# Kernel optimization log

Measured on AMD Instinct MI355X. Metric: run time of the kernel, lower is better.

## Reference

```python
import jax, jax.numpy as jnp
import numpy as np

B, T, D, H = 8, 1024, 768, 12
HD = D // H  # 64
EPS = 1e-5


def setup_inputs() -> dict:
    key = jax.random.key(0)
    ks = jax.random.split(key, 16)
    s = lambda fan_in: 1.0 / np.sqrt(fan_in)
    inp = {
        "x": jax.random.normal(ks[0], (B, T, D), jnp.float32),
        # per-head Q/K/V projections stacked: [H, D, HD]
        "wq": jax.random.normal(ks[1], (H, D, HD), jnp.float32) * s(D),
        "bq": jnp.zeros((H, HD), jnp.float32),
        "wk": jax.random.normal(ks[2], (H, D, HD), jnp.float32) * s(D),
        "bk": jnp.zeros((H, HD), jnp.float32),
        "wv": jax.random.normal(ks[3], (H, D, HD), jnp.float32) * s(D),
        "bv": jnp.zeros((H, HD), jnp.float32),
        "w_proj": jax.random.normal(ks[4], (D, D), jnp.float32) * s(D),
        "b_proj": jnp.zeros((D,), jnp.float32),
        "g1": jnp.ones((D,), jnp.float32),
        "be1": jnp.zeros((D,), jnp.float32),
        "g2": jnp.ones((D,), jnp.float32),
        "be2": jnp.zeros((D,), jnp.float32),
        "w_fc": jax.random.normal(ks[5], (D, 4 * D), jnp.float32) * s(D),
        "b_fc": jnp.zeros((4 * D,), jnp.float32),
        "w_cp": jax.random.normal(ks[6], (4 * D, D), jnp.float32) * s(4 * D),
        "b_cp": jnp.zeros((D,), jnp.float32),
    }
    return inp


def _layernorm(x, g, b):
    mu = jnp.mean(x, axis=-1, keepdims=True)
    var = jnp.var(x, axis=-1, keepdims=True)
    return (x - mu) * jax.lax.rsqrt(var + EPS) * g + b


def _block(x, wq, bq, wk, bk, wv, bv, w_proj, b_proj, g1, be1, g2, be2,
           w_fc, b_fc, w_cp, b_cp):
    # --- attention sublayer ---
    h = _layernorm(x, g1, be1)
    q = jnp.einsum('btd,hdk->bhtk', h, wq) + bq[None, :, None, :]
    k = jnp.einsum('btd,hdk->bhtk', h, wk) + bk[None, :, None, :]
    v = jnp.einsum('btd,hdk->bhtk', h, wv) + bv[None, :, None, :]
    scale = 1.0 / np.sqrt(HD)
    scores = jnp.einsum('bhqk,bhtk->bhqt', q, k) * scale  # [B,H,T,T]
    causal = jnp.tril(jnp.ones((T, T), bool))
    scores = jnp.where(causal, scores, jnp.finfo(scores.dtype).min)
    attn = jax.nn.softmax(scores, axis=-1)
    y = jnp.einsum('bhqt,bhtk->bhqk', attn, v)           # [B,H,T,HD]
    y = y.transpose(0, 2, 1, 3).reshape(x.shape[0], x.shape[1], D)
    x = x + y @ w_proj + b_proj
    # --- MLP sublayer ---
    h2 = _layernorm(x, g2, be2)
    h2 = jax.nn.gelu(h2 @ w_fc + b_fc, approximate=True)
    return x + h2 @ w_cp + b_cp


def reference(x, wq, bq, wk, bk, wv, bv, w_proj, b_proj, g1, be1, g2, be2,
              w_fc, b_fc, w_cp, b_cp):
    return _block(x, wq, bq, wk, bk, wv, bv, w_proj, b_proj, g1, be1,
                  g2, be2, w_fc, b_fc, w_cp, b_cp)
```

## Files before the change

### kernel.cpp

```cpp
#include <hip/hip_runtime.h>
#include <math.h>


typedef unsigned short ushort_t;
typedef __attribute__((ext_vector_type(8))) __bf16 bf16x8;
typedef __attribute__((ext_vector_type(4))) __bf16 bf16x4;
typedef __attribute__((ext_vector_type(4))) float floatx4;

__device__ __forceinline__ float bf2f(ushort_t u) {
  unsigned int x = ((unsigned int)u) << 16;
  return __builtin_bit_cast(float, x);
}
__device__ __forceinline__ ushort_t f2bf(float f) {
  unsigned int x = __builtin_bit_cast(unsigned int, f);
  unsigned int r = (x + 0x7FFFu + ((x >> 16) & 1u)) >> 16;
  return (ushort_t)r;
}

__global__ void __launch_bounds__(256) transpose_w(const float* __restrict__ in,
                                                   ushort_t* __restrict__ out,
                                                   int R, int C) {
  __shared__ ushort_t tl[64][65];
  int c0 = blockIdx.x * 64, r0 = blockIdx.y * 64;
  #pragma unroll
  for (int i = 0; i < 16; ++i) {
    int idx = threadIdx.x + i * 256;
    int r = idx >> 6, c = idx & 63;
    tl[c][r] = f2bf(in[(size_t)(r0 + r) * C + c0 + c]);
  }
  __syncthreads();
  #pragma unroll
  for (int i = 0; i < 16; ++i) {
    int idx = threadIdx.x + i * 256;
    int c = idx >> 6, r = idx & 63;
    out[(size_t)(c0 + c) * R + r0 + r] = tl[c][r];
  }
}

__global__ void __launch_bounds__(256) repack_qkv_t(const float* __restrict__ wq,
                                                    const float* __restrict__ wk,
                                                    const float* __restrict__ wv,
                                                    ushort_t* __restrict__ out) {
  __shared__ ushort_t tl[64][65];
  int s = blockIdx.y / 12, h = blockIdx.y % 12;
  const float* w = ((s == 0) ? wq : (s == 1) ? wk : wv) + (size_t)h * 768 * 64;
  int d0 = blockIdx.x * 64;
  #pragma unroll
  for (int i = 0; i < 16; ++i) {
    int idx = threadIdx.x + i * 256;
    int r = idx >> 6, c = idx & 63;
    tl[c][r] = f2bf(w[(size_t)(d0 + r) * 64 + c]);
  }
  __syncthreads();
  ushort_t* ob = out + (size_t)(s * 768 + h * 64) * 768;
  #pragma unroll
  for (int i = 0; i < 16; ++i) {
    int idx = threadIdx.x + i * 256;
    int c = idx >> 6, r = idx & 63;
    ob[(size_t)c * 768 + d0 + r] = tl[c][r];
  }
}

__global__ void __launch_bounds__(256) ln_kernel(const float* __restrict__ x,
                                                 const float* __restrict__ g,
                                                 const float* __restrict__ b,
                                                 ushort_t* __restrict__ out) {
  int row = blockIdx.x;
  int tid = threadIdx.x;
  const float* xr = x + (size_t)row * 768;
  float v0 = xr[tid], v1 = xr[tid + 256], v2 = xr[tid + 512];
  float s = v0 + v1 + v2;
  float s2 = v0 * v0 + v1 * v1 + v2 * v2;
  #pragma unroll
  for (int off = 32; off; off >>= 1) {
    s += __shfl_xor(s, off, 64);
    s2 += __shfl_xor(s2, off, 64);
  }
  __shared__ float ws1[4], ws2[4];
  int w = tid >> 6;
  if ((tid & 63) == 0) { ws1[w] = s; ws2[w] = s2; }
  __syncthreads();
  float S = ws1[0] + ws1[1] + ws1[2] + ws1[3];
  float S2 = ws2[0] + ws2[1] + ws2[2] + ws2[3];
  float mean = S * (1.0f / 768.0f);
  float var = S2 * (1.0f / 768.0f) - mean * mean;
  float rstd = rsqrtf(var + 1e-5f);
  ushort_t* orow = out + (size_t)row * 768;
  orow[tid]       = f2bf((v0 - mean) * rstd * g[tid]       + b[tid]);
  orow[tid + 256] = f2bf((v1 - mean) * rstd * g[tid + 256] + b[tid + 256]);
  orow[tid + 512] = f2bf((v2 - mean) * rstd * g[tid + 512] + b[tid + 512]);
}

enum { EPI_QKV = 0, EPI_RES = 1, EPI_FC = 2 };

template <int EPI>
__global__ void __launch_bounds__(256) gemm128(
    const ushort_t* __restrict__ A, const ushort_t* __restrict__ Bt,
    int M, int N, int K,
    const float* __restrict__ b0, const float* __restrict__ b1, const float* __restrict__ b2,
    const float* __restrict__ resid,
    ushort_t* __restrict__ ob0, ushort_t* __restrict__ ob1, ushort_t* __restrict__ ob2,
    float* __restrict__ of) {
  __shared__ __align__(16) ushort_t la[128 * 64];
  __shared__ __align__(16) ushort_t lb[128 * 64];
  int tid = threadIdx.x;
  int lane = tid & 63;
  int w = tid >> 6;
  int wr = w >> 1, wc = w & 1;
  int lm = lane & 15, q = lane >> 4;
  int m0 = blockIdx.x * 128, n0 = blockIdx.y * 128;

  const ushort_t* Ab = A + (size_t)m0 * K;
  const ushort_t* Bb = Bt + (size_t)n0 * K;

  floatx4 acc[4][4];
  #pragma unroll
  for (int i = 0; i < 4; ++i)
    #pragma unroll
    for (int j = 0; j < 4; ++j) acc[i][j] = (floatx4){0.f, 0.f, 0.f, 0.f};

  int srow = tid >> 3;
  int sch  = tid & 7;
  for (int k0 = 0; k0 < K; k0 += 64) {
    uint4 av0 = *reinterpret_cast<const uint4*>(Ab + (size_t)srow * K + k0 + sch * 8);
    uint4 av1 = *reinterpret_cast<const uint4*>(Ab + (size_t)(srow + 32) * K + k0 + sch * 8);
    uint4 av2 = *reinterpret_cast<const uint4*>(Ab + (size_t)(srow + 64) * K + k0 + sch * 8);
    uint4 av3 = *reinterpret_cast<const uint4*>(Ab + (size_t)(srow + 96) * K + k0 + sch * 8);
    uint4 bv0 = *reinterpret_cast<const uint4*>(Bb + (size_t)srow * K + k0 + sch * 8);
    uint4 bv1 = *reinterpret_cast<const uint4*>(Bb + (size_t)(srow + 32) * K + k0 + sch * 8);
    uint4 bv2 = *reinterpret_cast<const uint4*>(Bb + (size_t)(srow + 64) * K + k0 + sch * 8);
    uint4 bv3 = *reinterpret_cast<const uint4*>(Bb + (size_t)(srow + 96) * K + k0 + sch * 8);
    __syncthreads();
    *reinterpret_cast<uint4*>(&la[srow * 64 + ((sch ^ (srow & 7)) << 3)]) = av0;
    *reinterpret_cast<uint4*>(&la[(srow + 32) * 64 + ((sch ^ (srow & 7)) << 3)]) = av1;
    *reinterpret_cast<uint4*>(&la[(srow + 64) * 64 + ((sch ^ (srow & 7)) << 3)]) = av2;
    *reinterpret_cast<uint4*>(&la[(srow + 96) * 64 + ((sch ^ (srow & 7)) << 3)]) = av3;
    *reinterpret_cast<uint4*>(&lb[srow * 64 + ((sch ^ (srow & 7)) << 3)]) = bv0;
    *reinterpret_cast<uint4*>(&lb[(srow + 32) * 64 + ((sch ^ (srow & 7)) << 3)]) = bv1;
    *reinterpret_cast<uint4*>(&lb[(srow + 64) * 64 + ((sch ^ (srow & 7)) << 3)]) = bv2;
    *reinterpret_cast<uint4*>(&lb[(srow + 96) * 64 + ((sch ^ (srow & 7)) << 3)]) = bv3;
    __syncthreads();
    #pragma unroll
    for (int kk = 0; kk < 64; kk += 32) {
      int ch = (kk >> 3) + q;
      bf16x8 af[4], bfr[4];
      #pragma unroll
      for (int i = 0; i < 4; ++i) {
        int ra = wr * 64 + i * 16 + lm;
        int rb = wc * 64 + i * 16 + lm;
        af[i]  = *reinterpret_cast<const bf16x8*>(&la[ra * 64 + ((ch ^ (ra & 7)) << 3)]);
        bfr[i] = *reinterpret_cast<const bf16x8*>(&lb[rb * 64 + ((ch ^ (rb & 7)) << 3)]);
      }
      #pragma unroll
      for (int i = 0; i < 4; ++i)
        #pragma unroll
        for (int j = 0; j < 4; ++j)
          acc[i][j] = __builtin_amdgcn_mfma_f32_16x16x32_bf16(af[i], bfr[j], acc[i][j], 0, 0, 0);
    }
  }

  #pragma unroll
  for (int i = 0; i < 4; ++i) {
    #pragma unroll
    for (int j = 0; j < 4; ++j) {
      #pragma unroll
      for (int r = 0; r < 4; ++r) {
        float vacc = acc[i][j][r];
        int mm = m0 + wr * 64 + i * 16 + q * 4 + r;
        int nn = n0 + wc * 64 + j * 16 + lm;
        if constexpr (EPI == EPI_QKV) {
          int sel = nn / 768;
          int nq = nn - sel * 768;
          const float* bp = (sel == 0) ? b0 : (sel == 1) ? b1 : b2;
          ushort_t* dst = (sel == 0) ? ob0 : (sel == 1) ? ob1 : ob2;
          int bh = (mm >> 10) * 12 + (nq >> 6);
          size_t o = (size_t)bh * 65536 + (size_t)(mm & 1023) * 64 + (nq & 63);
          dst[o] = f2bf(vacc + bp[nq]);
        } else if constexpr (EPI == EPI_RES) {
          size_t o = (size_t)mm * 768 + nn;
          of[o] = vacc + b0[nn] + resid[o];
        } else {
          float u = vacc + b0[nn];
          float inner = 0.7978845608028654f * (u + 0.044715f * u * u * u);
          float e = __builtin_amdgcn_exp2f(inner * 2.885390081777927f);
          float gl = u - u / (e + 1.0f);
          ob0[(size_t)mm * 3072 + nn] = f2bf(gl);
        }
      }
    }
  }
}

__global__ void __launch_bounds__(256) transpose_v(const ushort_t* __restrict__ vb,
                                                   ushort_t* __restrict__ vt) {
  __shared__ ushort_t tl[64 * 72];
  int kt = blockIdx.x, bh = blockIdx.y;
  size_t base = (size_t)bh * 65536;
  int tid = threadIdx.x;
  #pragma unroll
  for (int i = 0; i < 2; ++i) {
    int r = (tid >> 3) + i * 32;
    int cb = (tid & 7) * 8;
    *reinterpret_cast<uint4*>(&tl[r * 72 + cb]) =
        *reinterpret_cast<const uint4*>(vb + base + (size_t)(kt * 64 + r) * 64 + cb);
  }
  __syncthreads();
  #pragma unroll
  for (int i = 0; i < 2; ++i) {
    int dim = (tid >> 3) + i * 32;
    int kb8 = (tid & 7) * 8;
    ushort_t tmp[8];
    #pragma unroll
    for (int j = 0; j < 8; ++j) tmp[j] = tl[(kb8 + j) * 72 + dim];
    *reinterpret_cast<uint4*>(vt + base + (size_t)dim * 1024 + kt * 64 + kb8) =
        *reinterpret_cast<uint4*>(tmp);
  }
}

__global__ void __launch_bounds__(256) attn_mfma(const ushort_t* __restrict__ qb,
                                                 const ushort_t* __restrict__ kb,
                                                 const ushort_t* __restrict__ vtb,
                                                 ushort_t* __restrict__ yb) {
  __shared__ __align__(16) ushort_t kl[64 * 72];
  __shared__ __align__(16) ushort_t vtl[64 * 72];
  int p = blockIdx.x;
  int bh = blockIdx.y;
  int tid = threadIdx.x, lane = tid & 63, w = tid >> 6;
  int col = lane & 15, quad = lane >> 4;
  size_t base = (size_t)bh * 65536;
  int b = bh / 12, h = bh - b * 12;
  const float sscale = 0.125f * 1.4426950408889634f;

  for (int phase = 0; phase < 2; ++phase) {
    int qt = (phase == 0) ? (15 - p) : p;
    int qw0 = qt * 64 + w * 16;
    int qg = qw0 + col;

    bf16x8 qf0 = *reinterpret_cast<const bf16x8*>(qb + base + (size_t)(qw0 + col) * 64 + quad * 8);
    bf16x8 qf1 = *reinterpret_cast<const bf16x8*>(qb + base + (size_t)(qw0 + col) * 64 + 32 + quad * 8);

    floatx4 O[4];
    #pragma unroll
    for (int ss = 0; ss < 4; ++ss) O[ss] = (floatx4){0.f, 0.f, 0.f, 0.f};
    float m = -INFINITY, l = 0.f;

    for (int kt0 = 0; kt0 <= qt * 64; kt0 += 64) {
      __syncthreads();
      #pragma unroll
      for (int i = 0; i < 2; ++i) {
        int r = (tid >> 3) + i * 32;
        int cb = (tid & 7) * 8;
        *reinterpret_cast<uint4*>(&kl[r * 72 + cb]) =
            *reinterpret_cast<const uint4*>(kb + base + (size_t)(kt0 + r) * 64 + cb);
        *reinterpret_cast<uint4*>(&vtl[r * 72 + cb]) =
            *reinterpret_cast<const uint4*>(vtb + base + (size_t)r * 1024 + kt0 + cb);
      }
      __syncthreads();
      int nk = qw0 + 16 - kt0;
      if (nk > 64) nk = 64;
      int ng = (nk + 31) >> 5;
      for (int g = 0; g < ng; ++g) {
        int ksA = kt0 + g * 32;
        int ksB = ksA + 16;
        int rbase = (g * 32 + col) * 72;
        bf16x8 kfA0 = *reinterpret_cast<const bf16x8*>(&kl[rbase + quad * 8]);
        bf16x8 kfA1 = *reinterpret_cast<const bf16x8*>(&kl[rbase + 32 + quad * 8]);
        bf16x8 kfB0 = *reinterpret_cast<const bf16x8*>(&kl[rbase + 16 * 72 + quad * 8]);
        bf16x8 kfB1 = *reinterpret_cast<const bf16x8*>(&kl[rbase + 16 * 72 + 32 + quad * 8]);
        floatx4 saA = (floatx4){0.f, 0.f, 0.f, 0.f};
        floatx4 saB = (floatx4){0.f, 0.f, 0.f, 0.f};
        __builtin_amdgcn_s_setprio(1);
        saA = __builtin_amdgcn_mfma_f32_16x16x32_bf16(kfA0, qf0, saA, 0, 0, 0);
        saA = __builtin_amdgcn_mfma_f32_16x16x32_bf16(kfA1, qf1, saA, 0, 0, 0);
        saB = __builtin_amdgcn_mfma_f32_16x16x32_bf16(kfB0, qf0, saB, 0, 0, 0);
        saB = __builtin_amdgcn_mfma_f32_16x16x32_bf16(kfB1, qf1, saB, 0, 0, 0);
        __builtin_amdgcn_s_setprio(0);
        float s0 = saA[0] * sscale, s1 = saA[1] * sscale;
        float s2 = saA[2] * sscale, s3 = saA[3] * sscale;
        float s4 = saB[0] * sscale, s5 = saB[1] * sscale;
        float s6 = saB[2] * sscale, s7 = saB[3] * sscale;
        if (ksA + 15 > qw0) {
          int keyb = ksA + quad * 4;
          if (keyb + 0 > qg) s0 = -3.0e38f;
          if (keyb + 1 > qg) s1 = -3.0e38f;
          if (keyb + 2 > qg) s2 = -3.0e38f;
          if (keyb + 3 > qg) s3 = -3.0e38f;
        }
        if (ksB + 15 > qw0) {
          int keyb = ksB + quad * 4;
          if (keyb + 0 > qg) s4 = -3.0e38f;
          if (keyb + 1 > qg) s5 = -3.0e38f;
          if (keyb + 2 > qg) s6 = -3.0e38f;
          if (keyb + 3 > qg) s7 = -3.0e38f;
        }
        float mloc = fmaxf(fmaxf(fmaxf(s0, s1), fmaxf(s2, s3)),
                           fmaxf(fmaxf(s4, s5), fmaxf(s6, s7)));
        mloc = fmaxf(mloc, __shfl_xor(mloc, 16, 64));
        mloc = fmaxf(mloc, __shfl_xor(mloc, 32, 64));
        float mnew = fmaxf(m, mloc);
        float c = __builtin_amdgcn_exp2f(m - mnew);
        float p0 = __builtin_amdgcn_exp2f(s0 - mnew);
        float p1 = __builtin_amdgcn_exp2f(s1 - mnew);
        float p2 = __builtin_amdgcn_exp2f(s2 - mnew);
        float p3 = __builtin_amdgcn_exp2f(s3 - mnew);
        float p4 = __builtin_amdgcn_exp2f(s4 - mnew);
        float p5 = __builtin_amdgcn_exp2f(s5 - mnew);
        float p6 = __builtin_amdgcn_exp2f(s6 - mnew);
        float p7 = __builtin_amdgcn_exp2f(s7 - mnew);
        float ll = ((p0 + p1) + (p2 + p3)) + ((p4 + p5) + (p6 + p7));
        ll += __shfl_xor(ll, 16, 64);
        ll += __shfl_xor(ll, 32, 64);
        l = l * c + ll;
        m = mnew;
        float c0 = __shfl(c, quad * 4 + 0, 64);
        float c1 = __shfl(c, quad * 4 + 1, 64);
        float c2 = __shfl(c, quad * 4 + 2, 64);
        float c3 = __shfl(c, quad * 4 + 3, 64);
        bf16x8 pf = {(__bf16)p0, (__bf16)p1, (__bf16)p2, (__bf16)p3,
                     (__bf16)p4, (__bf16)p5, (__bf16)p6, (__bf16)p7};
        __builtin_amdgcn_s_setprio(1);
        #pragma unroll
        for (int ss = 0; ss < 4; ++ss) {
          O[ss][0] *= c0; O[ss][1] *= c1; O[ss][2] *= c2; O[ss][3] *= c3;
          int vrow = (ss * 16 + col) * 72 + g * 32 + quad * 4;
          bf16x4 va = *reinterpret_cast<const bf16x4*>(&vtl[vrow]);
          bf16x4 vb = *reinterpret_cast<const bf16x4*>(&vtl[vrow + 16]);
          bf16x8 vf = {va[0], va[1], va[2], va[3], vb[0], vb[1], vb[2], vb[3]};
          O[ss] = __builtin_amdgcn_mfma_f32_16x16x32_bf16(pf, vf, O[ss], 0, 0, 0);
        }
        __builtin_amdgcn_s_setprio(0);
      }
    }

    float linv = 1.0f / l;
    float l0 = __shfl(linv, quad * 4 + 0, 64);
    float l1 = __shfl(linv, quad * 4 + 1, 64);
    float l2 = __shfl(linv, quad * 4 + 2, 64);
    float l3 = __shfl(linv, quad * 4 + 3, 64);
    #pragma unroll
    for (int ss = 0; ss < 4; ++ss) {
      float lr[4] = {l0, l1, l2, l3};
      #pragma unroll
      for (int r = 0; r < 4; ++r) {
        int t = qw0 + quad * 4 + r;
        yb[((size_t)(b * 1024 + t)) * 768 + h * 64 + ss * 16 + col] = f2bf(O[ss][r] * lr[r]);
      }
    }
  }
}

extern "C" void kernel_launch(void* const* d_in, const int* in_sizes, int n_in,
                              void* d_out, int out_size, void* d_ws, size_t ws_size,
                              hipStream_t stream) {
  const float* x      = (const float*)d_in[0];
  const float* wq     = (const float*)d_in[1];
  const float* bq     = (const float*)d_in[2];
  const float* wk     = (const float*)d_in[3];
  const float* bk     = (const float*)d_in[4];
  const float* wv     = (const float*)d_in[5];
  const float* bv     = (const float*)d_in[6];
  const float* w_proj = (const float*)d_in[7];
  const float* b_proj = (const float*)d_in[8];
  const float* g1     = (const float*)d_in[9];
  const float* be1    = (const float*)d_in[10];
  const float* g2     = (const float*)d_in[11];
  const float* be2    = (const float*)d_in[12];
  const float* w_fc   = (const float*)d_in[13];
  const float* b_fc   = (const float*)d_in[14];
  const float* w_cp   = (const float*)d_in[15];
  const float* b_cp   = (const float*)d_in[16];
  float* out = (float*)d_out;

  char* ws = (char*)d_ws;
  size_t off = 0;
  auto alloc = [&](size_t bytes) -> char* {
    char* p = ws + off;
    off += (bytes + 255) & ~(size_t)255;
    return p;
  };
  const size_t MD = 8192ull * 768;
  ushort_t* wqkvT  = (ushort_t*)alloc(2304ull * 768 * 2);
  ushort_t* wprojT = (ushort_t*)alloc(768ull * 768 * 2);
  ushort_t* wfcT   = (ushort_t*)alloc(3072ull * 768 * 2);
  ushort_t* wcpT   = (ushort_t*)alloc(768ull * 3072 * 2);
  ushort_t* hbuf   = (ushort_t*)alloc(MD * 2);
  ushort_t* qbuf   = (ushort_t*)alloc(MD * 2);
  ushort_t* kbuf   = (ushort_t*)alloc(MD * 2);
  ushort_t* vbuf   = (ushort_t*)alloc(MD * 2);
  ushort_t* ybuf   = (ushort_t*)alloc(MD * 2);
  float*    x1     = (float*)alloc(MD * 4);
  ushort_t* h2buf  = (ushort_t*)alloc(MD * 2);
  ushort_t* vtbuf  = hbuf;
  ushort_t* fcbuf  = qbuf;

  repack_qkv_t<<<dim3(12, 36), 256, 0, stream>>>(wq, wk, wv, wqkvT);
  transpose_w<<<dim3(12, 12), 256, 0, stream>>>(w_proj, wprojT, 768, 768);
  transpose_w<<<dim3(48, 12), 256, 0, stream>>>(w_fc, wfcT, 768, 3072);
  transpose_w<<<dim3(12, 48), 256, 0, stream>>>(w_cp, wcpT, 3072, 768);

  ln_kernel<<<8192, 256, 0, stream>>>(x, g1, be1, hbuf);
  gemm128<EPI_QKV><<<dim3(64, 18), 256, 0, stream>>>(
      hbuf, wqkvT, 8192, 2304, 768, bq, bk, bv, nullptr, qbuf, kbuf, vbuf, nullptr);
  transpose_v<<<dim3(16, 96), 256, 0, stream>>>(vbuf, vtbuf);
  attn_mfma<<<dim3(8, 96), 256, 0, stream>>>(qbuf, kbuf, vtbuf, ybuf);
  gemm128<EPI_RES><<<dim3(64, 6), 256, 0, stream>>>(
      ybuf, wprojT, 8192, 768, 768, b_proj, nullptr, nullptr, x,
      nullptr, nullptr, nullptr, x1);
  ln_kernel<<<8192, 256, 0, stream>>>(x1, g2, be2, h2buf);
  gemm128<EPI_FC><<<dim3(64, 24), 256, 0, stream>>>(
      h2buf, wfcT, 8192, 3072, 768, b_fc, nullptr, nullptr, nullptr,
      fcbuf, nullptr, nullptr, nullptr);
  gemm128<EPI_RES><<<dim3(64, 6), 256, 0, stream>>>(
      fcbuf, wcpT, 8192, 768, 3072, b_cp, nullptr, nullptr, x1,
      nullptr, nullptr, nullptr, out);
}
```

Before: 406.4 us.

## Process both paired query tiles in one pass sharing K/V tile loads

```diff
diff --git a/kernel.cpp b/kernel.cpp
--- a/kernel.cpp
+++ b/kernel.cpp
@@ -223,116 +223,188 @@
                                                  ushort_t* __restrict__ yb) {
   __shared__ __align__(16) ushort_t kl[64 * 72];
   __shared__ __align__(16) ushort_t vtl[64 * 72];
-  int p = blockIdx.x;
-  int bh = blockIdx.y;
+  int id = blockIdx.x;
+  int p = id / 96, bh = id - p * 96;
+  int qtA = 15 - p, qtB = p;
   int tid = threadIdx.x, lane = tid & 63, w = tid >> 6;
   int col = lane & 15, quad = lane >> 4;
+  int qw0A = qtA * 64 + w * 16, qw0B = qtB * 64 + w * 16;
+  int qgA = qw0A + col, qgB = qw0B + col;
   size_t base = (size_t)bh * 65536;
   int b = bh / 12, h = bh - b * 12;
   const float sscale = 0.125f * 1.4426950408889634f;
 
-  for (int phase = 0; phase < 2; ++phase) {
-    int qt = (phase == 0) ? (15 - p) : p;
-    int qw0 = qt * 64 + w * 16;
-    int qg = qw0 + col;
-
-    bf16x8 qf0 = *reinterpret_cast<const bf16x8*>(qb + base + (size_t)(qw0 + col) * 64 + quad * 8);
-    bf16x8 qf1 = *reinterpret_cast<const bf16x8*>(qb + base + (size_t)(qw0 + col) * 64 + 32 + quad * 8);
-
-    floatx4 O[4];
-    #pragma unroll
-    for (int ss = 0; ss < 4; ++ss) O[ss] = (floatx4){0.f, 0.f, 0.f, 0.f};
-    float m = -INFINITY, l = 0.f;
-
-    for (int kt0 = 0; kt0 <= qt * 64; kt0 += 64) {
-      __syncthreads();
-      #pragma unroll
-      for (int i = 0; i < 2; ++i) {
-        int r = (tid >> 3) + i * 32;
-        int cb = (tid & 7) * 8;
-        *reinterpret_cast<uint4*>(&kl[r * 72 + cb]) =
-            *reinterpret_cast<const uint4*>(kb + base + (size_t)(kt0 + r) * 64 + cb);
-        *reinterpret_cast<uint4*>(&vtl[r * 72 + cb]) =
-            *reinterpret_cast<const uint4*>(vtb + base + (size_t)r * 1024 + kt0 + cb);
-      }
-      __syncthreads();
-      int nk = qw0 + 16 - kt0;
-      if (nk > 64) nk = 64;
-      int ng = (nk + 31) >> 5;
-      for (int g = 0; g < ng; ++g) {
-        int ksA = kt0 + g * 32;
-        int ksB = ksA + 16;
-        int rbase = (g * 32 + col) * 72;
-        bf16x8 kfA0 = *reinterpret_cast<const bf16x8*>(&kl[rbase + quad * 8]);
-        bf16x8 kfA1 = *reinterpret_cast<const bf16x8*>(&kl[rbase + 32 + quad * 8]);
-        bf16x8 kfB0 = *reinterpret_cast<const bf16x8*>(&kl[rbase + 16 * 72 + quad * 8]);
-        bf16x8 kfB1 = *reinterpret_cast<const bf16x8*>(&kl[rbase + 16 * 72 + 32 + quad * 8]);
-        floatx4 saA = (floatx4){0.f, 0.f, 0.f, 0.f};
-        floatx4 saB = (floatx4){0.f, 0.f, 0.f, 0.f};
-        __builtin_amdgcn_s_setprio(1);
-        saA = __builtin_amdgcn_mfma_f32_16x16x32_bf16(kfA0, qf0, saA, 0, 0, 0);
-        saA = __builtin_amdgcn_mfma_f32_16x16x32_bf16(kfA1, qf1, saA, 0, 0, 0);
-        saB = __builtin_amdgcn_mfma_f32_16x16x32_bf16(kfB0, qf0, saB, 0, 0, 0);
-        saB = __builtin_amdgcn_mfma_f32_16x16x32_bf16(kfB1, qf1, saB, 0, 0, 0);
-        __builtin_amdgcn_s_setprio(0);
-        float s0 = saA[0] * sscale, s1 = saA[1] * sscale;
-        float s2 = saA[2] * sscale, s3 = saA[3] * sscale;
-        float s4 = saB[0] * sscale, s5 = saB[1] * sscale;
-        float s6 = saB[2] * sscale, s7 = saB[3] * sscale;
-        if (ksA + 15 > qw0) {
-          int keyb = ksA + quad * 4;
-          if (keyb + 0 > qg) s0 = -3.0e38f;
-          if (keyb + 1 > qg) s1 = -3.0e38f;
-          if (keyb + 2 > qg) s2 = -3.0e38f;
-          if (keyb + 3 > qg) s3 = -3.0e38f;
-        }
-        if (ksB + 15 > qw0) {
-          int keyb = ksB + quad * 4;
-          if (keyb + 0 > qg) s4 = -3.0e38f;
-          if (keyb + 1 > qg) s5 = -3.0e38f;
-          if (keyb + 2 > qg) s6 = -3.0e38f;
-          if (keyb + 3 > qg) s7 = -3.0e38f;
-        }
-        float mloc = fmaxf(fmaxf(fmaxf(s0, s1), fmaxf(s2, s3)),
-                           fmaxf(fmaxf(s4, s5), fmaxf(s6, s7)));
+  bf16x8 qfA0 = *reinterpret_cast<const bf16x8*>(qb + base + (size_t)(qw0A + col) * 64 + quad * 8);
+  bf16x8 qfA1 = *reinterpret_cast<const bf16x8*>(qb + base + (size_t)(qw0A + col) * 64 + 32 + quad * 8);
+  bf16x8 qfB0 = *reinterpret_cast<const bf16x8*>(qb + base + (size_t)(qw0B + col) * 64 + quad * 8);
+  bf16x8 qfB1 = *reinterpret_cast<const bf16x8*>(qb + base + (size_t)(qw0B + col) * 64 + 32 + quad * 8);
+
+  floatx4 OA[4], OB[4];
+  #pragma unroll
+  for (int ss = 0; ss < 4; ++ss) {
+    OA[ss] = (floatx4){0.f, 0.f, 0.f, 0.f};
+    OB[ss] = (floatx4){0.f, 0.f, 0.f, 0.f};
+  }
+  float mA = -INFINITY, lA = 0.f, mB = -INFINITY, lB = 0.f;
+
+  for (int kt0 = 0; kt0 <= qtA * 64; kt0 += 64) {
+    __syncthreads();
+    #pragma unroll
+    for (int i = 0; i < 2; ++i) {
+      int r = (tid >> 3) + i * 32;
+      int cb = (tid & 7) * 8;
+      *reinterpret_cast<uint4*>(&kl[r * 72 + cb]) =
+          *reinterpret_cast<const uint4*>(kb + base + (size_t)(kt0 + r) * 64 + cb);
+      *reinterpret_cast<uint4*>(&vtl[r * 72 + cb]) =
+          *reinterpret_cast<const uint4*>(vtb + base + (size_t)r * 1024 + kt0 + cb);
+    }
+    __syncthreads();
+    bool bAct = (kt0 <= qtB * 64);
+    int ngA = (kt0 == qtA * 64) ? ((w * 16 + 16 + 31) >> 5) : 2;
+    int ngB = !bAct ? 0 : ((kt0 == qtB * 64) ? ((w * 16 + 16 + 31) >> 5) : 2);
+    int ng = ngA > ngB ? ngA : ngB;
+    for (int g = 0; g < ng; ++g) {
+      bool doA = g < ngA, doB = g < ngB;
+      int ks0 = kt0 + g * 32, ks1 = ks0 + 16;
+      int rbase = (g * 32 + col) * 72;
+      bf16x8 kf00 = *reinterpret_cast<const bf16x8*>(&kl[rbase + quad * 8]);
+      bf16x8 kf01 = *reinterpret_cast<const bf16x8*>(&kl[rbase + 32 + quad * 8]);
+      bf16x8 kf10 = *reinterpret_cast<const bf16x8*>(&kl[rbase + 16 * 72 + quad * 8]);
+      bf16x8 kf11 = *reinterpret_cast<const bf16x8*>(&kl[rbase + 16 * 72 + 32 + quad * 8]);
+      floatx4 sA0 = (floatx4){0.f, 0.f, 0.f, 0.f};
+      floatx4 sA1 = (floatx4){0.f, 0.f, 0.f, 0.f};
+      floatx4 sB0 = (floatx4){0.f, 0.f, 0.f, 0.f};
+      floatx4 sB1 = (floatx4){0.f, 0.f, 0.f, 0.f};
+      __builtin_amdgcn_s_setprio(1);
+      if (doA) {
+        sA0 = __builtin_amdgcn_mfma_f32_16x16x32_bf16(kf00, qfA0, sA0, 0, 0, 0);
+        sA0 = __builtin_amdgcn_mfma_f32_16x16x32_bf16(kf01, qfA1, sA0, 0, 0, 0);
+        sA1 = __builtin_amdgcn_mfma_f32_16x16x32_bf16(kf10, qfA0, sA1, 0, 0, 0);
+        sA1 = __builtin_amdgcn_mfma_f32_16x16x32_bf16(kf11, qfA1, sA1, 0, 0, 0);
+      }
+      if (doB) {
+        sB0 = __builtin_amdgcn_mfma_f32_16x16x32_bf16(kf00, qfB0, sB0, 0, 0, 0);
+        sB0 = __builtin_amdgcn_mfma_f32_16x16x32_bf16(kf01, qfB1, sB0, 0, 0, 0);
+        sB1 = __builtin_amdgcn_mfma_f32_16x16x32_bf16(kf10, qfB0, sB1, 0, 0, 0);
+        sB1 = __builtin_amdgcn_mfma_f32_16x16x32_bf16(kf11, qfB1, sB1, 0, 0, 0);
+      }
+      __builtin_amdgcn_s_setprio(0);
+      float c0A = 1.f, c1A = 1.f, c2A = 1.f, c3A = 1.f;
+      bf16x8 pfA;
+      if (doA) {
+        float a0 = sA0[0] * sscale, a1 = sA0[1] * sscale;
+        float a2 = sA0[2] * sscale, a3 = sA0[3] * sscale;
+        float a4 = sA1[0] * sscale, a5 = sA1[1] * sscale;
+        float a6 = sA1[2] * sscale, a7 = sA1[3] * sscale;
+        if (ks0 + 15 > qw0A) {
+          int keyb = ks0 + quad * 4;
+          if (keyb + 0 > qgA) a0 = -3.0e38f;
+          if (keyb + 1 > qgA) a1 = -3.0e38f;
+          if (keyb + 2 > qgA) a2 = -3.0e38f;
+          if (keyb + 3 > qgA) a3 = -3.0e38f;
+        }
+        if (ks1 + 15 > qw0A) {
+          int keyb = ks1 + quad * 4;
+          if (keyb + 0 > qgA) a4 = -3.0e38f;
+          if (keyb + 1 > qgA) a5 = -3.0e38f;
+          if (keyb + 2 > qgA) a6 = -3.0e38f;
+          if (keyb + 3 > qgA) a7 = -3.0e38f;
+        }
+        float mloc = fmaxf(fmaxf(fmaxf(a0, a1), fmaxf(a2, a3)),
+                           fmaxf(fmaxf(a4, a5), fmaxf(a6, a7)));
         mloc = fmaxf(mloc, __shfl_xor(mloc, 16, 64));
         mloc = fmaxf(mloc, __shfl_xor(mloc, 32, 64));
-        float mnew = fmaxf(m, mloc);
-        float c = __builtin_amdgcn_exp2f(m - mnew);
-        float p0 = __builtin_amdgcn_exp2f(s0 - mnew);
-        float p1 = __builtin_amdgcn_exp2f(s1 - mnew);
-        float p2 = __builtin_amdgcn_exp2f(s2 - mnew);
-        float p3 = __builtin_amdgcn_exp2f(s3 - mnew);
-        float p4 = __builtin_amdgcn_exp2f(s4 - mnew);
-        float p5 = __builtin_amdgcn_exp2f(s5 - mnew);
-        float p6 = __builtin_amdgcn_exp2f(s6 - mnew);
-        float p7 = __builtin_amdgcn_exp2f(s7 - mnew);
+        float mnew = fmaxf(mA, mloc);
+        float c = __builtin_amdgcn_exp2f(mA - mnew);
+        float p0 = __builtin_amdgcn_exp2f(a0 - mnew);
+        float p1 = __builtin_amdgcn_exp2f(a1 - mnew);
+        float p2 = __builtin_amdgcn_exp2f(a2 - mnew);
+        float p3 = __builtin_amdgcn_exp2f(a3 - mnew);
+        float p4 = __builtin_amdgcn_exp2f(a4 - mnew);
+        float p5 = __builtin_amdgcn_exp2f(a5 - mnew);
+        float p6 = __builtin_amdgcn_exp2f(a6 - mnew);
+        float p7 = __builtin_amdgcn_exp2f(a7 - mnew);
         float ll = ((p0 + p1) + (p2 + p3)) + ((p4 + p5) + (p6 + p7));
         ll += __shfl_xor(ll, 16, 64);
         ll += __shfl_xor(ll, 32, 64);
-        l = l * c + ll;
-        m = mnew;
-        float c0 = __shfl(c, quad * 4 + 0, 64);
-        float c1 = __shfl(c, quad * 4 + 1, 64);
-        float c2 = __shfl(c, quad * 4 + 2, 64);
-        float c3 = __shfl(c, quad * 4 + 3, 64);
-        bf16x8 pf = {(__bf16)p0, (__bf16)p1, (__bf16)p2, (__bf16)p3,
+        lA = lA * c + ll;
+        mA = mnew;
+        c0A = __shfl(c, quad * 4 + 0, 64);
+        c1A = __shfl(c, quad * 4 + 1, 64);
+        c2A = __shfl(c, quad * 4 + 2, 64);
+        c3A = __shfl(c, quad * 4 + 3, 64);
+        pfA = bf16x8{(__bf16)p0, (__bf16)p1, (__bf16)p2, (__bf16)p3,
                      (__bf16)p4, (__bf16)p5, (__bf16)p6, (__bf16)p7};
-        __builtin_amdgcn_s_setprio(1);
-        #pragma unroll
-        for (int ss = 0; ss < 4; ++ss) {
-          O[ss][0] *= c0; O[ss][1] *= c1; O[ss][2] *= c2; O[ss][3] *= c3;
-          int vrow = (ss * 16 + col) * 72 + g * 32 + quad * 4;
-          bf16x4 va = *reinterpret_cast<const bf16x4*>(&vtl[vrow]);
-          bf16x4 vb = *reinterpret_cast<const bf16x4*>(&vtl[vrow + 16]);
-          bf16x8 vf = {va[0], va[1], va[2], va[3], vb[0], vb[1], vb[2], vb[3]};
-          O[ss] = __builtin_amdgcn_mfma_f32_16x16x32_bf16(pf, vf, O[ss], 0, 0, 0);
-        }
-        __builtin_amdgcn_s_setprio(0);
-      }
+      }
+      float c0B = 1.f, c1B = 1.f, c2B = 1.f, c3B = 1.f;
+      bf16x8 pfB;
+      if (doB) {
+        float a0 = sB0[0] * sscale, a1 = sB0[1] * sscale;
+        float a2 = sB0[2] * sscale, a3 = sB0[3] * sscale;
+        float a4 = sB1[0] * sscale, a5 = sB1[1] * sscale;
+        float a6 = sB1[2] * sscale, a7 = sB1[3] * sscale;
+        if (ks0 + 15 > qw0B) {
+          int keyb = ks0 + quad * 4;
+          if (keyb + 0 > qgB) a0 = -3.0e38f;
+          if (keyb + 1 > qgB) a1 = -3.0e38f;
+          if (keyb + 2 > qgB) a2 = -3.0e38f;
+          if (keyb + 3 > qgB) a3 = -3.0e38f;
+        }
+        if (ks1 + 15 > qw0B) {
+          int keyb = ks1 + quad * 4;
+          if (keyb + 0 > qgB) a4 = -3.0e38f;
+          if (keyb + 1 > qgB) a5 = -3.0e38f;
+          if (keyb + 2 > qgB) a6 = -3.0e38f;
+          if (keyb + 3 > qgB) a7 = -3.0e38f;
+        }
+        float mloc = fmaxf(fmaxf(fmaxf(a0, a1), fmaxf(a2, a3)),
+                           fmaxf(fmaxf(a4, a5), fmaxf(a6, a7)));
+        mloc = fmaxf(mloc, __shfl_xor(mloc, 16, 64));
+        mloc = fmaxf(mloc, __shfl_xor(mloc, 32, 64));
+        float mnew = fmaxf(mB, mloc);
+        float c = __builtin_amdgcn_exp2f(mB - mnew);
+        float p0 = __builtin_amdgcn_exp2f(a0 - mnew);
+        float p1 = __builtin_amdgcn_exp2f(a1 - mnew);
+        float p2 = __builtin_amdgcn_exp2f(a2 - mnew);
+        float p3 = __builtin_amdgcn_exp2f(a3 - mnew);
+        float p4 = __builtin_amdgcn_exp2f(a4 - mnew);
+        float p5 = __builtin_amdgcn_exp2f(a5 - mnew);
+        float p6 = __builtin_amdgcn_exp2f(a6 - mnew);
+        float p7 = __builtin_amdgcn_exp2f(a7 - mnew);
+        float ll = ((p0 + p1) + (p2 + p3)) + ((p4 + p5) + (p6 + p7));
+        ll += __shfl_xor(ll, 16, 64);
+        ll += __shfl_xor(ll, 32, 64);
+        lB = lB * c + ll;
+        mB = mnew;
+        c0B = __shfl(c, quad * 4 + 0, 64);
+        c1B = __shfl(c, quad * 4 + 1, 64);
+        c2B = __shfl(c, quad * 4 + 2, 64);
+        c3B = __shfl(c, quad * 4 + 3, 64);
+        pfB = bf16x8{(__bf16)p0, (__bf16)p1, (__bf16)p2, (__bf16)p3,
+                     (__bf16)p4, (__bf16)p5, (__bf16)p6, (__bf16)p7};
+      }
+      __builtin_amdgcn_s_setprio(1);
+      #pragma unroll
+      for (int ss = 0; ss < 4; ++ss) {
+        int vrow = (ss * 16 + col) * 72 + g * 32 + quad * 4;
+        bf16x4 va = *reinterpret_cast<const bf16x4*>(&vtl[vrow]);
+        bf16x4 vb = *reinterpret_cast<const bf16x4*>(&vtl[vrow + 16]);
+        bf16x8 vf = {va[0], va[1], va[2], va[3], vb[0], vb[1], vb[2], vb[3]};
+        if (doA) {
+          OA[ss][0] *= c0A; OA[ss][1] *= c1A; OA[ss][2] *= c2A; OA[ss][3] *= c3A;
+          OA[ss] = __builtin_amdgcn_mfma_f32_16x16x32_bf16(pfA, vf, OA[ss], 0, 0, 0);
+        }
+        if (doB) {
+          OB[ss][0] *= c0B; OB[ss][1] *= c1B; OB[ss][2] *= c2B; OB[ss][3] *= c3B;
+          OB[ss] = __builtin_amdgcn_mfma_f32_16x16x32_bf16(pfB, vf, OB[ss], 0, 0, 0);
+        }
+      }
+      __builtin_amdgcn_s_setprio(0);
     }
-
-    float linv = 1.0f / l;
+  }
+
+  {
+    float linv = 1.0f / lA;
     float l0 = __shfl(linv, quad * 4 + 0, 64);
     float l1 = __shfl(linv, quad * 4 + 1, 64);
     float l2 = __shfl(linv, quad * 4 + 2, 64);
@@ -342,8 +414,24 @@
       float lr[4] = {l0, l1, l2, l3};
       #pragma unroll
       for (int r = 0; r < 4; ++r) {
-        int t = qw0 + quad * 4 + r;
-        yb[((size_t)(b * 1024 + t)) * 768 + h * 64 + ss * 16 + col] = f2bf(O[ss][r] * lr[r]);
+        int t = qw0A + quad * 4 + r;
+        yb[((size_t)(b * 1024 + t)) * 768 + h * 64 + ss * 16 + col] = f2bf(OA[ss][r] * lr[r]);
+      }
+    }
+  }
+  {
+    float linv = 1.0f / lB;
+    float l0 = __shfl(linv, quad * 4 + 0, 64);
+    float l1 = __shfl(linv, quad * 4 + 1, 64);
+    float l2 = __shfl(linv, quad * 4 + 2, 64);
+    float l3 = __shfl(linv, quad * 4 + 3, 64);
+    #pragma unroll
+    for (int ss = 0; ss < 4; ++ss) {
+      float lr[4] = {l0, l1, l2, l3};
+      #pragma unroll
+      for (int r = 0; r < 4; ++r) {
+        int t = qw0B + quad * 4 + r;
+        yb[((size_t)(b * 1024 + t)) * 768 + h * 64 + ss * 16 + col] = f2bf(OB[ss][r] * lr[r]);
       }
     }
   }
@@ -402,7 +490,7 @@
   gemm128<EPI_QKV><<<dim3(64, 18), 256, 0, stream>>>(
       hbuf, wqkvT, 8192, 2304, 768, bq, bk, bv, nullptr, qbuf, kbuf, vbuf, nullptr);
   transpose_v<<<dim3(16, 96), 256, 0, stream>>>(vbuf, vtbuf);
-  attn_mfma<<<dim3(8, 96), 256, 0, stream>>>(qbuf, kbuf, vtbuf, ybuf);
+  attn_mfma<<<768, 256, 0, stream>>>(qbuf, kbuf, vtbuf, ybuf);
   gemm128<EPI_RES><<<dim3(64, 6), 256, 0, stream>>>(
       ybuf, wprojT, 8192, 768, 768, b_proj, nullptr, nullptr, x,
       nullptr, nullptr, nullptr, x1);
```

Measured after the change: 421.0 us. +3.6%, slower.

## Shrink GEMM M-tile to 64 and XOR-swizzle attention K/V shared memory

Applied to the files above, without the earlier changes.

```diff
diff --git a/kernel.cpp b/kernel.cpp
--- a/kernel.cpp
+++ b/kernel.cpp
@@ -94,28 +94,28 @@
 enum { EPI_QKV = 0, EPI_RES = 1, EPI_FC = 2 };
 
 template <int EPI>
-__global__ void __launch_bounds__(256) gemm128(
+__global__ void __launch_bounds__(256) gemm64t(
     const ushort_t* __restrict__ A, const ushort_t* __restrict__ Bt,
     int M, int N, int K,
     const float* __restrict__ b0, const float* __restrict__ b1, const float* __restrict__ b2,
     const float* __restrict__ resid,
     ushort_t* __restrict__ ob0, ushort_t* __restrict__ ob1, ushort_t* __restrict__ ob2,
     float* __restrict__ of) {
-  __shared__ __align__(16) ushort_t la[128 * 64];
+  __shared__ __align__(16) ushort_t la[64 * 64];
   __shared__ __align__(16) ushort_t lb[128 * 64];
   int tid = threadIdx.x;
   int lane = tid & 63;
   int w = tid >> 6;
   int wr = w >> 1, wc = w & 1;
   int lm = lane & 15, q = lane >> 4;
-  int m0 = blockIdx.x * 128, n0 = blockIdx.y * 128;
+  int m0 = blockIdx.x * 64, n0 = blockIdx.y * 128;
 
   const ushort_t* Ab = A + (size_t)m0 * K;
   const ushort_t* Bb = Bt + (size_t)n0 * K;
 
-  floatx4 acc[4][4];
-  #pragma unroll
-  for (int i = 0; i < 4; ++i)
+  floatx4 acc[2][4];
+  #pragma unroll
+  for (int i = 0; i < 2; ++i)
     #pragma unroll
     for (int j = 0; j < 4; ++j) acc[i][j] = (floatx4){0.f, 0.f, 0.f, 0.f};
 
@@ -124,8 +124,6 @@
   for (int k0 = 0; k0 < K; k0 += 64) {
     uint4 av0 = *reinterpret_cast<const uint4*>(Ab + (size_t)srow * K + k0 + sch * 8);
     uint4 av1 = *reinterpret_cast<const uint4*>(Ab + (size_t)(srow + 32) * K + k0 + sch * 8);
-    uint4 av2 = *reinterpret_cast<const uint4*>(Ab + (size_t)(srow + 64) * K + k0 + sch * 8);
-    uint4 av3 = *reinterpret_cast<const uint4*>(Ab + (size_t)(srow + 96) * K + k0 + sch * 8);
     uint4 bv0 = *reinterpret_cast<const uint4*>(Bb + (size_t)srow * K + k0 + sch * 8);
     uint4 bv1 = *reinterpret_cast<const uint4*>(Bb + (size_t)(srow + 32) * K + k0 + sch * 8);
     uint4 bv2 = *reinterpret_cast<const uint4*>(Bb + (size_t)(srow + 64) * K + k0 + sch * 8);
@@ -133,8 +131,6 @@
     __syncthreads();
     *reinterpret_cast<uint4*>(&la[srow * 64 + ((sch ^ (srow & 7)) << 3)]) = av0;
     *reinterpret_cast<uint4*>(&la[(srow + 32) * 64 + ((sch ^ (srow & 7)) << 3)]) = av1;
-    *reinterpret_cast<uint4*>(&la[(srow + 64) * 64 + ((sch ^ (srow & 7)) << 3)]) = av2;
-    *reinterpret_cast<uint4*>(&la[(srow + 96) * 64 + ((sch ^ (srow & 7)) << 3)]) = av3;
     *reinterpret_cast<uint4*>(&lb[srow * 64 + ((sch ^ (srow & 7)) << 3)]) = bv0;
     *reinterpret_cast<uint4*>(&lb[(srow + 32) * 64 + ((sch ^ (srow & 7)) << 3)]) = bv1;
     *reinterpret_cast<uint4*>(&lb[(srow + 64) * 64 + ((sch ^ (srow & 7)) << 3)]) = bv2;
@@ -143,16 +139,19 @@
     #pragma unroll
     for (int kk = 0; kk < 64; kk += 32) {
       int ch = (kk >> 3) + q;
-      bf16x8 af[4], bfr[4];
+      bf16x8 af[2], bfr[4];
       #pragma unroll
-      for (int i = 0; i < 4; ++i) {
-        int ra = wr * 64 + i * 16 + lm;
-        int rb = wc * 64 + i * 16 + lm;
+      for (int i = 0; i < 2; ++i) {
+        int ra = wr * 32 + i * 16 + lm;
         af[i]  = *reinterpret_cast<const bf16x8*>(&la[ra * 64 + ((ch ^ (ra & 7)) << 3)]);
-        bfr[i] = *reinterpret_cast<const bf16x8*>(&lb[rb * 64 + ((ch ^ (rb & 7)) << 3)]);
       }
       #pragma unroll
-      for (int i = 0; i < 4; ++i)
+      for (int j = 0; j < 4; ++j) {
+        int rb = wc * 64 + j * 16 + lm;
+        bfr[j] = *reinterpret_cast<const bf16x8*>(&lb[rb * 64 + ((ch ^ (rb & 7)) << 3)]);
+      }
+      #pragma unroll
+      for (int i = 0; i < 2; ++i)
         #pragma unroll
         for (int j = 0; j < 4; ++j)
           acc[i][j] = __builtin_amdgcn_mfma_f32_16x16x32_bf16(af[i], bfr[j], acc[i][j], 0, 0, 0);
@@ -160,13 +159,13 @@
   }
 
   #pragma unroll
-  for (int i = 0; i < 4; ++i) {
+  for (int i = 0; i < 2; ++i) {
     #pragma unroll
     for (int j = 0; j < 4; ++j) {
       #pragma unroll
       for (int r = 0; r < 4; ++r) {
         float vacc = acc[i][j][r];
-        int mm = m0 + wr * 64 + i * 16 + q * 4 + r;
+        int mm = m0 + wr * 32 + i * 16 + q * 4 + r;
         int nn = n0 + wc * 64 + j * 16 + lm;
         if constexpr (EPI == EPI_QKV) {
           int sel = nn / 768;
@@ -221,8 +220,8 @@
                                                  const ushort_t* __restrict__ kb,
                                                  const ushort_t* __restrict__ vtb,
                                                  ushort_t* __restrict__ yb) {
-  __shared__ __align__(16) ushort_t kl[64 * 72];
-  __shared__ __align__(16) ushort_t vtl[64 * 72];
+  __shared__ __align__(16) ushort_t kl[64 * 64];
+  __shared__ __align__(16) ushort_t vtl[64 * 64];
   int p = blockIdx.x;
   int bh = blockIdx.y;
   int tid = threadIdx.x, lane = tid & 63, w = tid >> 6;
@@ -246,14 +245,19 @@
 
     for (int kt0 = 0; kt0 <= qt * 64; kt0 += 64) {
       __syncthreads();
-      #pragma unroll
-      for (int i = 0; i < 2; ++i) {
-        int r = (tid >> 3) + i * 32;
-        int cb = (tid & 7) * 8;
-        *reinterpret_cast<uint4*>(&kl[r * 72 + cb]) =
-            *reinterpret_cast<const uint4*>(kb + base + (size_t)(kt0 + r) * 64 + cb);
-        *reinterpret_cast<uint4*>(&vtl[r * 72 + cb]) =
-            *reinterpret_cast<const uint4*>(vtb + base + (size_t)r * 1024 + kt0 + cb);
+      {
+        int r0 = tid >> 3;
+        int cb = tid & 7;
+        int sw = (cb ^ (r0 & 7)) << 3;
+        *reinterpret_cast<uint4*>(&kl[r0 * 64 + sw]) =
+            *reinterpret_cast<const uint4*>(kb + base + (size_t)(kt0 + r0) * 64 + cb * 8);
+        *reinterpret_cast<uint4*>(&vtl[r0 * 64 + sw]) =
+            *reinterpret_cast<const uint4*>(vtb + base + (size_t)r0 * 1024 + kt0 + cb * 8);
+        int r1 = r0 + 32;
+        *reinterpret_cast<uint4*>(&kl[r1 * 64 + sw]) =
+            *reinterpret_cast<const uint4*>(kb + base + (size_t)(kt0 + r1) * 64 + cb * 8);
+        *reinterpret_cast<uint4*>(&vtl[r1 * 64 + sw]) =
+            *reinterpret_cast<const uint4*>(vtb + base + (size_t)r1 * 1024 + kt0 + cb * 8);
       }
       __syncthreads();
       int nk = qw0 + 16 - kt0;
@@ -262,11 +266,14 @@
       for (int g = 0; g < ng; ++g) {
         int ksA = kt0 + g * 32;
         int ksB = ksA + 16;
-        int rbase = (g * 32 + col) * 72;
-        bf16x8 kfA0 = *reinterpret_cast<const bf16x8*>(&kl[rbase + quad * 8]);
-        bf16x8 kfA1 = *reinterpret_cast<const bf16x8*>(&kl[rbase + 32 + quad * 8]);
-        bf16x8 kfB0 = *reinterpret_cast<const bf16x8*>(&kl[rbase + 16 * 72 + quad * 8]);
-        bf16x8 kfB1 = *reinterpret_cast<const bf16x8*>(&kl[rbase + 16 * 72 + 32 + quad * 8]);
+        int rowA = g * 32 + col;
+        int rxa = rowA & 7;
+        int sa = rowA * 64;
+        int sb = sa + 16 * 64;
+        bf16x8 kfA0 = *reinterpret_cast<const bf16x8*>(&kl[sa + ((quad ^ rxa) << 3)]);
+        bf16x8 kfA1 = *reinterpret_cast<const bf16x8*>(&kl[sa + (((4 + quad) ^ rxa) << 3)]);
+        bf16x8 kfB0 = *reinterpret_cast<const bf16x8*>(&kl[sb + ((quad ^ rxa) << 3)]);
+        bf16x8 kfB1 = *reinterpret_cast<const bf16x8*>(&kl[sb + (((4 + quad) ^ rxa) << 3)]);
         floatx4 saA = (floatx4){0.f, 0.f, 0.f, 0.f};
         floatx4 saB = (floatx4){0.f, 0.f, 0.f, 0.f};
         __builtin_amdgcn_s_setprio(1);
@@ -322,9 +329,13 @@
         #pragma unroll
         for (int ss = 0; ss < 4; ++ss) {
           O[ss][0] *= c0; O[ss][1] *= c1; O[ss][2] *= c2; O[ss][3] *= c3;
-          int vrow = (ss * 16 + col) * 72 + g * 32 + quad * 4;
-          bf16x4 va = *reinterpret_cast<const bf16x4*>(&vtl[vrow]);
-          bf16x4 vb = *reinterpret_cast<const bf16x4*>(&vtl[vrow + 16]);
+          int vd = ss * 16 + col;
+          int vbase = vd * 64;
+          int vx = vd & 7;
+          int ca = g * 4 + (quad >> 1);
+          int ia = (quad & 1) * 4;
+          bf16x4 va = *reinterpret_cast<const bf16x4*>(&vtl[vbase + ((ca ^ vx) << 3) + ia]);
+          bf16x4 vb = *reinterpret_cast<const bf16x4*>(&vtl[vbase + (((ca + 2) ^ vx) << 3) + ia]);
           bf16x8 vf = {va[0], va[1], va[2], va[3], vb[0], vb[1], vb[2], vb[3]};
           O[ss] = __builtin_amdgcn_mfma_f32_16x16x32_bf16(pf, vf, O[ss], 0, 0, 0);
         }
@@ -399,18 +410,18 @@
   transpose_w<<<dim3(12, 48), 256, 0, stream>>>(w_cp, wcpT, 3072, 768);
 
   ln_kernel<<<8192, 256, 0, stream>>>(x, g1, be1, hbuf);
-  gemm128<EPI_QKV><<<dim3(64, 18), 256, 0, stream>>>(
+  gemm64t<EPI_QKV><<<dim3(128, 18), 256, 0, stream>>>(
       hbuf, wqkvT, 8192, 2304, 768, bq, bk, bv, nullptr, qbuf, kbuf, vbuf, nullptr);
   transpose_v<<<dim3(16, 96), 256, 0, stream>>>(vbuf, vtbuf);
   attn_mfma<<<dim3(8, 96), 256, 0, stream>>>(qbuf, kbuf, vtbuf, ybuf);
-  gemm128<EPI_RES><<<dim3(64, 6), 256, 0, stream>>>(
+  gemm64t<EPI_RES><<<dim3(128, 6), 256, 0, stream>>>(
       ybuf, wprojT, 8192, 768, 768, b_proj, nullptr, nullptr, x,
       nullptr, nullptr, nullptr, x1);
   ln_kernel<<<8192, 256, 0, stream>>>(x1, g2, be2, h2buf);
-  gemm128<EPI_FC><<<dim3(64, 24), 256, 0, stream>>>(
+  gemm64t<EPI_FC><<<dim3(128, 24), 256, 0, stream>>>(
       h2buf, wfcT, 8192, 3072, 768, b_fc, nullptr, nullptr, nullptr,
       fcbuf, nullptr, nullptr, nullptr);
-  gemm128<EPI_RES><<<dim3(64, 6), 256, 0, stream>>>(
+  gemm64t<EPI_RES><<<dim3(128, 6), 256, 0, stream>>>(
       fcbuf, wcpT, 8192, 768, 3072, b_cp, nullptr, nullptr, x1,
       nullptr, nullptr, nullptr, out);
 }
```

Result: faster. 388.5 us (-4.4%).
